# Kernel tuning notes

Measured on AMD Instinct MI355X. Metric: run time of the kernel, lower is better.

## Reference

```python
import jax, jax.numpy as jnp
import numpy as np
import math

# Module constants derived from init_kwargs
DIM1, DIM2 = 32, 32          # n_patches = (512//16, 512//16)
PREFIX = 8                   # num_prefix_tokens
STD = 5.0                    # gauss_std
NUM_HEADS = 12               # orig_attn.num_heads (ViT-B)
EMBED_DIM = 768


def gaussian_window(n1, n2, std):
    # torch linspace(start*c, (start+(n-1))*c, n) == (arange(n)-(n-1)/2)*c
    c = 1.0 / (std * math.sqrt(2.0))
    k1 = (jnp.arange(n1, dtype=jnp.float32) - (n1 - 1) / 2.0) * c
    k2 = (jnp.arange(n2, dtype=jnp.float32) - (n2 - 1) / 2.0) * c
    return jnp.exp(-(k1[:, None] ** 2 + k2[None, :] ** 2))


def attn_addition():
    # Same-padding cross-correlation of per-token delta images with the window
    # collapses to: add[(i,l),(p,q)] = window[i-p+DIM1-1, l-q+DIM2-1]
    win = gaussian_window(2 * DIM1 - 1, 2 * DIM2 - 1, STD)
    i = jnp.arange(DIM1)
    l = jnp.arange(DIM2)
    di = i[:, None] - i[None, :] + (DIM1 - 1)   # [i, p]
    dl = l[:, None] - l[None, :] + (DIM2 - 1)   # [l, q]
    add = win[di[:, None, :, None], dl[None, :, None, :]]  # [i, l, p, q]
    add = add.reshape(DIM1 * DIM2, DIM1 * DIM2)
    # zero rows/cols for prefix tokens (prepended)
    return jnp.pad(add, ((PREFIX, 0), (PREFIX, 0)))


def setup_inputs() -> dict:
    key = jax.random.key(0)
    ks = jax.random.split(key, 5)
    B, N, C = 8, DIM1 * DIM2 + PREFIX, EMBED_DIM
    return {
        "x": jax.random.normal(ks[0], (B, N, C), dtype=jnp.float32),
        "qkv_w": jax.random.normal(ks[1], (3 * C, C), dtype=jnp.float32) * 0.02,
        "qkv_b": jax.random.normal(ks[2], (3 * C,), dtype=jnp.float32) * 0.02,
        "proj_w": jax.random.normal(ks[3], (C, C), dtype=jnp.float32) * 0.02,
        "proj_b": jax.random.normal(ks[4], (C,), dtype=jnp.float32) * 0.02,
    }


def reference(x, qkv_w, qkv_b, proj_w, proj_b):
    B, N, C = x.shape
    H = NUM_HEADS
    hd = C // H
    scale = hd ** (-0.5)
    add = attn_addition()  # [N, N] constant bias

    qkv = x @ qkv_w.T + qkv_b                      # [B, N, 3C]
    q, k, v = jnp.split(qkv, 3, axis=-1)           # q computed but unused (k.k^T attention)
    k = k.reshape(B, N, H, hd)
    v = v.reshape(B, N, H, hd)

    attn = jnp.einsum("bihd,bjhd->bhij", k, k) * scale + add[None, None]
    attn = jax.nn.softmax(attn, axis=-1)
    out = jnp.einsum("bhij,bjhd->bihd", attn, v).reshape(B, N, C)
    out = out @ proj_w.T + proj_b
    return out
```

## Files before the change

### kernel.cpp

```cpp
#include <hip/hip_runtime.h>
#include <stdint.h>

typedef __bf16 bf16;
typedef _Float16 f16;
typedef __bf16 bf16x8 __attribute__((ext_vector_type(8)));
typedef __bf16 bf16x4 __attribute__((ext_vector_type(4)));
typedef float f32x4 __attribute__((ext_vector_type(4)));

#define NSEQ 1032
#define BATCH 8
#define NHEADS 12
#define HD 64
#define CDIM 768
#define MROWS (BATCH * NSEQ)
#define PREFIX 8
#define NJT 17
#define NQ16 72
#define KSTRIDE 1152
#define VSTRIDE 1152
#define KSCALE 0.42466090f

__device__ __forceinline__ unsigned short f2bf_rne(float f) {
    union { float f; uint32_t u; } v; v.f = f;
    uint32_t u = v.u;
    return (unsigned short)((u + 0x7fffu + ((u >> 16) & 1u)) >> 16);
}

__device__ __forceinline__ void gload_lds16(const bf16* g, bf16* l) {
    __builtin_amdgcn_global_load_lds(
        (const __attribute__((address_space(1))) void*)g,
        (__attribute__((address_space(3))) void*)l, 16, 0, 0);
}

__device__ __forceinline__ void cast4(const float* src, bf16* dst, int i) {
    float4 f = ((const float4*)src)[i];
    ushort4 o;
    o.x = f2bf_rne(f.x); o.y = f2bf_rne(f.y);
    o.z = f2bf_rne(f.z); o.w = f2bf_rne(f.w);
    ((ushort4*)dst)[i] = o;
}

__device__ __forceinline__ void bar() {
    asm volatile("s_waitcnt lgkmcnt(0)" ::: "memory");
    __builtin_amdgcn_s_barrier();
    asm volatile("" ::: "memory");
}

#define VMBAR(N) do { \
        asm volatile("s_waitcnt vmcnt(" #N ")" ::: "memory"); \
        __builtin_amdgcn_s_barrier(); \
        asm volatile("" ::: "memory"); \
    } while (0)

__global__ void prep_kernel(const float* __restrict__ x,
                            const float* __restrict__ wkv,
                            const float* __restrict__ pw,
                            bf16* __restrict__ x_bf, bf16* __restrict__ wkv_bf,
                            bf16* __restrict__ pw_bf, float* __restrict__ Bias,
                            bf16* __restrict__ k_bf, bf16* __restrict__ vt_bf) {
    const int N0 = NQ16 * NJT * 1024;
    const int N1 = MROWS * CDIM / 4;
    const int N2 = 2 * CDIM * CDIM / 4;
    const int N3 = CDIM * CDIM / 4;
    const int N4 = BATCH * NHEADS * 120 * 8;
    const int N5 = BATCH * NHEADS * 64 * 15;
    int i = blockIdx.x * blockDim.x + threadIdx.x;
    if (i < N0) {
        int r    = i & 3;
        int l15  = (i >> 2) & 15;
        int quad = (i >> 6) & 3;
        int kt   = (i >> 8) & 3;
        int rest = i >> 10;
        int q16  = rest / NJT;
        int jt   = rest - q16 * NJT;
        int q = q16 * 16 + l15;
        int k = jt * 64 + kt * 16 + quad * 4 + r;
        float v;
        if (k >= NSEQ) v = -65504.f;
        else if (q < PREFIX || q >= NSEQ || k < PREFIX) v = 0.f;
        else {
            int rp = q - PREFIX, cp = k - PREFIX;
            int d1 = (rp >> 5) - (cp >> 5);
            int d2 = (rp & 31) - (cp & 31);
            v = 1.44269504f * __expf(-0.02f * (float)(d1 * d1 + d2 * d2));
        }
        Bias[i] = v;
        return;
    }
    i -= N0;
    if (i < N1) { cast4(x, x_bf, i); return; }
    i -= N1;
    if (i < N2) { cast4(wkv, wkv_bf, i); return; }
    i -= N2;
    if (i < N3) { cast4(pw, pw_bf, i); return; }
    i -= N3;
    if (i < N4) {
        int bh = i / 960, rem = i - bh * 960;
        int row = 1032 + (rem >> 3), ch = rem & 7;
        uint4 z = {0u, 0u, 0u, 0u};
        *(uint4*)&k_bf[((size_t)bh * KSTRIDE + row) * HD + ch * 8] = z;
        return;
    }
    i -= N4;
    if (i < N5) {
        int bh = i / 960, rem = i - bh * 960;
        int d = rem / 15, ch = rem - d * 15;
        uint4 z = {0u, 0u, 0u, 0u};
        *(uint4*)&vt_bf[((size_t)bh * HD + d) * VSTRIDE + 1032 + ch * 8] = z;
    }
}

template<int EPI>
__global__ __launch_bounds__(512) void gemm_nt(
    const bf16* __restrict__ A, const bf16* __restrict__ B,
    const float* __restrict__ bias,
    float* __restrict__ Cout, bf16* __restrict__ Kout, bf16* __restrict__ Vout,
    int M, int N, int K)
{
    __shared__ bf16 sA[2][256 * 32];
    __shared__ bf16 sB[2][128 * 32];
    const int t = threadIdx.x;
    const int w = t >> 6;
    const int l = t & 63;
    const int quad = l >> 4;
    const int l15 = l & 15;
    const int wy = w >> 1, wx = w & 1;

    const int nbx = gridDim.x;
    int id = blockIdx.y * nbx + blockIdx.x;
    {
        int nwg = nbx * gridDim.y;
        int qq = nwg >> 3, rr = nwg & 7;
        int xcd = id & 7, idx = id >> 3;
        id = (xcd < rr) ? (xcd * (qq + 1) + idx)
                        : (rr * (qq + 1) + (xcd - rr) * qq + idx);
    }
    const int m0 = (id / nbx) * 256;
    const int n0 = (id % nbx) * 128;
    const int co = (quad ^ ((l15 >> 1) & 3)) * 8;

    int r0 = t >> 2;            int c0 = (t & 3) ^ ((r0 >> 1) & 3);
    int r1 = 128 + (t >> 2);    int c1 = (t & 3) ^ ((r1 >> 1) & 3);
    int rB = t >> 2;            int cB = (t & 3) ^ ((rB >> 1) & 3);
    int ra0 = m0 + r0; if (ra0 >= M) ra0 = M - 1;
    int ra1 = m0 + r1; if (ra1 >= M) ra1 = M - 1;
    const bf16* gA0 = A + (size_t)ra0 * K + c0 * 8;
    const bf16* gA1 = A + (size_t)ra1 * K + c1 * 8;
    const bf16* gB0 = B + (size_t)(n0 + rB) * K + cB * 8;
    const int oA0 = (w * 64) * 8;
    const int oA1 = (512 + w * 64) * 8;
    const int oB0 = (w * 64) * 8;

    f32x4 acc[4][4] = {};

#define STAGE(BUF) do { \
        gload_lds16(gA0, &sA[BUF][oA0]); gload_lds16(gA1, &sA[BUF][oA1]); \
        gload_lds16(gB0, &sB[BUF][oB0]); \
        gA0 += 32; gA1 += 32; gB0 += 32; \
    } while (0)

#define COMPUTE(BUF) do { \
        bf16x8 af_[4], bq_[4]; \
        _Pragma("unroll") \
        for (int mt = 0; mt < 4; ++mt) \
            af_[mt] = *(const bf16x8*)&sA[BUF][(wy*64 + mt*16 + l15) * 32 + co]; \
        _Pragma("unroll") \
        for (int nt = 0; nt < 4; ++nt) \
            bq_[nt] = *(const bf16x8*)&sB[BUF][(wx*64 + nt*16 + l15) * 32 + co]; \
        _Pragma("unroll") \
        for (int mt = 0; mt < 4; ++mt) \
            _Pragma("unroll") \
            for (int nt = 0; nt < 4; ++nt) \
                acc[mt][nt] = __builtin_amdgcn_mfma_f32_16x16x32_bf16( \
                    af_[mt], bq_[nt], acc[mt][nt], 0, 0, 0); \
    } while (0)

    const int NT = K / 32;
    STAGE(0);
    STAGE(1);
    VMBAR(3);

    #pragma unroll 1
    for (int p = 0; p <= NT - 4; p += 2) {
        COMPUTE(0);
        bar();
        STAGE(0);
        VMBAR(3);
        COMPUTE(1);
        bar();
        STAGE(1);
        VMBAR(3);
    }
    COMPUTE(0);
    VMBAR(0);
    COMPUTE(1);
#undef STAGE
#undef COMPUTE

    if (EPI == 0) {
        #pragma unroll
        for (int mt = 0; mt < 4; ++mt) {
            #pragma unroll
            for (int r = 0; r < 4; ++r) {
                int m = m0 + wy*64 + mt*16 + quad*4 + r;
                if (m >= M) continue;
                #pragma unroll
                for (int nt = 0; nt < 4; ++nt) {
                    int n = n0 + wx*64 + nt*16 + l15;
                    Cout[(size_t)m * N + n] = acc[mt][nt][r] + bias[n];
                }
            }
        }
    } else {
        #pragma unroll
        for (int mt = 0; mt < 4; ++mt) {
            int mb = m0 + wy*64 + mt*16 + quad*4;
            if (mb >= M) continue;
            int b = mb / NSEQ, s = mb % NSEQ;
            #pragma unroll
            for (int nt = 0; nt < 4; ++nt) {
                int n = n0 + wx*64 + nt*16 + l15;
                float bn = bias[n];
                if (n < CDIM) {
                    int h = n >> 6, d = n & 63;
                    bf16* kp = &Kout[(((size_t)(b*NHEADS + h))*KSTRIDE + s)*HD + d];
                    #pragma unroll
                    for (int r = 0; r < 4; ++r)
                        kp[(size_t)r * HD] = (bf16)((acc[mt][nt][r] + bn) * KSCALE);
                } else {
                    int n2 = n - CDIM;
                    int h = n2 >> 6, d = n2 & 63;
                    bf16x4 pv = { (bf16)(acc[mt][nt][0] + bn), (bf16)(acc[mt][nt][1] + bn),
                                  (bf16)(acc[mt][nt][2] + bn), (bf16)(acc[mt][nt][3] + bn) };
                    *(bf16x4*)&Vout[(((size_t)(b*NHEADS + h))*HD + d)*VSTRIDE + s] = pv;
                }
            }
        }
    }
}

__global__ __launch_bounds__(512) void attn_kernel(
    const bf16* __restrict__ Kbuf, const bf16* __restrict__ VTbuf,
    const float* __restrict__ Bias, bf16* __restrict__ Hout)
{
    const int bh = blockIdx.x;
    const int b = bh / NHEADS, h = bh % NHEADS;
    const int q0 = blockIdx.y * 128;
    const bf16* Kh  = Kbuf  + (size_t)bh * KSTRIDE * HD;
    const bf16* VTh = VTbuf + (size_t)bh * HD * VSTRIDE;

    __shared__ bf16 sK[2][64 * 64];
    __shared__ bf16 sVT[2][64 * 64];
    __shared__ bf16 sP[128 * 64];

    const int t = threadIdx.x;
    const int w = t >> 6, l = t & 63, quad = l >> 4, l15 = l & 15;
    const int sw = l15 & 7;

    const int r0 = t >> 3, c0 = t & 7;
    const int dk0 = r0*64 + ((c0 ^ (r0 & 7)) << 3);

    const bf16* pK0 = Kh + (size_t)r0 * HD + c0 * 8;
    const bf16* pV0 = VTh + (size_t)r0 * VSTRIDE + c0 * 8;
    const float* pB = Bias + (size_t)(blockIdx.y*8 + w) * NJT * 1024 + quad*64 + l15*4;

    bf16x8 qf[2];
    {
        int row = q0 + w*16 + l15;
        #pragma unroll
        for (int ks = 0; ks < 2; ++ks)
            qf[ks] = *(const bf16x8*)&Kh[(size_t)row * HD + ks*32 + quad*8];
    }

    bf16x8 onesb;
    #pragma unroll
    for (int e = 0; e < 8; ++e) onesb[e] = (bf16)1.0f;

    f32x4 Oacc[4] = {};
    f32x4 Lacc = {};
    const int sPr0 = (w*16 + l15) * 64;

    uint4 kva, vva;
    f32x4 bpA[4], bpB[4];

#define PREFETCH_KV() do { \
        kva = *(const uint4*)pK0; \
        vva = *(const uint4*)pV0; \
        pK0 += 64*HD; pV0 += 64; \
    } while (0)

#define PREFETCH_B(BANK) do { \
        _Pragma("unroll") \
        for (int kt = 0; kt < 4; ++kt) \
            BANK[kt] = *(const f32x4*)(pB + kt*256); \
        pB += 1024; \
    } while (0)

#define ITER(CUR, ACC, NEXT) do { \
        *(uint4*)&sK[CUR][dk0] = kva; \
        *(uint4*)&sVT[CUR][dk0] = vva; \
        PREFETCH_KV(); \
        PREFETCH_B(NEXT); \
        bar(); \
        _Pragma("unroll") \
        for (int ks = 0; ks < 2; ++ks) { \
            bf16x8 af[4]; \
            _Pragma("unroll") \
            for (int kt = 0; kt < 4; ++kt) \
                af[kt] = *(const bf16x8*)&sK[CUR][(kt*16 + l15)*64 + (((ks*4 + quad) ^ sw) << 3)]; \
            __builtin_amdgcn_s_setprio(1); \
            _Pragma("unroll") \
            for (int kt = 0; kt < 4; ++kt) \
                ACC[kt] = __builtin_amdgcn_mfma_f32_16x16x32_bf16( \
                    af[kt], qf[ks], ACC[kt], 0, 0, 0); \
            __builtin_amdgcn_s_setprio(0); \
        } \
        _Pragma("unroll") \
        for (int kt = 0; kt < 4; ++kt) { \
            float p0 = __builtin_exp2f(ACC[kt][0]); \
            float p1 = __builtin_exp2f(ACC[kt][1]); \
            float p2 = __builtin_exp2f(ACC[kt][2]); \
            float p3 = __builtin_exp2f(ACC[kt][3]); \
            bf16x4 pv = { (bf16)p0, (bf16)p1, (bf16)p2, (bf16)p3 }; \
            int g = (kt*2 + (quad >> 1)) ^ sw; \
            *(bf16x4*)&sP[sPr0 + g*8 + (quad & 1)*4] = pv; \
        } \
        _Pragma("unroll") \
        for (int ks = 0; ks < 2; ++ks) { \
            bf16x8 bv[4]; \
            _Pragma("unroll") \
            for (int dt = 0; dt < 4; ++dt) \
                bv[dt] = *(const bf16x8*)&sVT[CUR][(dt*16 + l15)*64 + (((ks*4 + quad) ^ sw) << 3)]; \
            __builtin_amdgcn_s_setprio(1); \
            bf16x8 ap = *(const bf16x8*)&sP[sPr0 + (((ks*4 + quad) ^ sw) * 8)]; \
            _Pragma("unroll") \
            for (int dt = 0; dt < 4; ++dt) \
                Oacc[dt] = __builtin_amdgcn_mfma_f32_16x16x32_bf16( \
                    ap, bv[dt], Oacc[dt], 0, 0, 0); \
            Lacc = __builtin_amdgcn_mfma_f32_16x16x32_bf16( \
                ap, onesb, Lacc, 0, 0, 0); \
            __builtin_amdgcn_s_setprio(0); \
        } \
    } while (0)

    PREFETCH_KV();
    PREFETCH_B(bpA);
    ITER(0, bpA, bpB);
    #pragma unroll 1
    for (int it = 0; it < (NJT - 1) / 2; ++it) {
        ITER(1, bpB, bpA);
        ITER(0, bpA, bpB);
    }
#undef ITER
#undef PREFETCH_KV
#undef PREFETCH_B

    #pragma unroll
    for (int r = 0; r < 4; ++r) {
        int g = q0 + w*16 + quad*4 + r;
        if (g >= NSEQ) continue;
        float inv = 1.f / Lacc[r];
        size_t base = ((size_t)(b * NSEQ) + g) * CDIM + h * HD;
        #pragma unroll
        for (int dt = 0; dt < 4; ++dt)
            Hout[base + dt*16 + l15] = (bf16)(Oacc[dt][r] * inv);
    }
}

extern "C" void kernel_launch(void* const* d_in, const int* in_sizes, int n_in,
                              void* d_out, int out_size, void* d_ws, size_t ws_size,
                              hipStream_t stream) {
    const float* x      = (const float*)d_in[0];
    const float* qkv_w  = (const float*)d_in[1];
    const float* qkv_b  = (const float*)d_in[2];
    const float* proj_w = (const float*)d_in[3];
    const float* proj_b = (const float*)d_in[4];
    float* out = (float*)d_out;

    char* ws = (char*)d_ws;
    const size_t XBF_BYTES   = (size_t)MROWS * CDIM * 2;
    const size_t WKV_BYTES   = (size_t)2 * CDIM * CDIM * 2;
    const size_t PW_BYTES    = (size_t)CDIM * CDIM * 2;
    const size_t BIAS_BYTES  = (size_t)NQ16 * NJT * 1024 * 4;
    const size_t KBF_BYTES   = (size_t)BATCH * NHEADS * KSTRIDE * HD * 2;

    bf16*  x_bf   = (bf16*)ws;
    bf16*  wkv_bf = (bf16*)(ws + XBF_BYTES);
    bf16*  pw_bf  = (bf16*)(ws + XBF_BYTES + WKV_BYTES);
    float* bias_t = (float*)(ws + XBF_BYTES + WKV_BYTES + PW_BYTES);
    bf16*  k_bf   = (bf16*)(ws + XBF_BYTES + WKV_BYTES + PW_BYTES + BIAS_BYTES);
    bf16*  vt_bf  = (bf16*)(ws + XBF_BYTES + WKV_BYTES + PW_BYTES + BIAS_BYTES + KBF_BYTES);

    {
        int total = NQ16 * NJT * 1024 + MROWS * CDIM / 4
                  + 2 * CDIM * CDIM / 4 + CDIM * CDIM / 4
                  + BATCH * NHEADS * 120 * 8 + BATCH * NHEADS * 64 * 15;
        prep_kernel<<<dim3((total + 255) / 256), dim3(256), 0, stream>>>(
            x, qkv_w + (size_t)CDIM * CDIM, proj_w, x_bf, wkv_bf, pw_bf, bias_t,
            k_bf, vt_bf);
    }

    {
        dim3 grid(1536 / 128, (MROWS + 255) / 256);
        gemm_nt<1><<<grid, dim3(512), 0, stream>>>(x_bf, wkv_bf, qkv_b + CDIM,
                                                   nullptr, k_bf, vt_bf,
                                                   MROWS, 1536, CDIM);
    }

    {
        dim3 grid(BATCH * NHEADS, 9);
        attn_kernel<<<grid, dim3(512), 0, stream>>>(k_bf, vt_bf, bias_t, x_bf);
    }

    {
        dim3 grid(CDIM / 128, (MROWS + 255) / 256);
        gemm_nt<0><<<grid, dim3(512), 0, stream>>>(x_bf, pw_bf, proj_b,
                                                   out, nullptr, nullptr,
                                                   MROWS, CDIM, CDIM);
    }
}
```

Measured before the change: 200.9 us.

## Rewrite attention with 32x32 MFMA, register-resident P, fp16 bias, async LDS staging

Rewrites the attention kernel so each of four waves owns 32 query rows and uses 32x32x16 bf16 MFMAs. The softmax probabilities are packed to bf16 and rearranged with permlane32 swaps, so they stay in registers instead of round-tripping through shared memory. K/V tiles are now staged with direct global-to-LDS loads, double-buffered, replacing register prefetch and LDS stores. The precomputed bias table is stored as fp16 in the new accumulator layout, halving its bandwidth at some precision cost. Block size drops from 512 to 256 threads.

New measurement: 210.8 us. 1.05x slower.

```diff
diff --git a/kernel.cpp b/kernel.cpp
--- a/kernel.cpp
+++ b/kernel.cpp
@@ -6,6 +6,10 @@
 typedef __bf16 bf16x8 __attribute__((ext_vector_type(8)));
 typedef __bf16 bf16x4 __attribute__((ext_vector_type(4)));
 typedef float f32x4 __attribute__((ext_vector_type(4)));
+typedef float f32x16 __attribute__((ext_vector_type(16)));
+typedef _Float16 f16x8 __attribute__((ext_vector_type(8)));
+typedef unsigned int u32x4 __attribute__((ext_vector_type(4)));
+typedef unsigned int uint2v __attribute__((ext_vector_type(2)));
 
 #define NSEQ 1032
 #define BATCH 8
@@ -15,7 +19,7 @@
 #define MROWS (BATCH * NSEQ)
 #define PREFIX 8
 #define NJT 17
-#define NQ16 72
+#define NQ32 36
 #define KSTRIDE 1152
 #define VSTRIDE 1152
 #define KSCALE 0.42466090f
@@ -30,6 +34,12 @@
     __builtin_amdgcn_global_load_lds(
         (const __attribute__((address_space(1))) void*)g,
         (__attribute__((address_space(3))) void*)l, 16, 0, 0);
+}
+
+__device__ __forceinline__ unsigned cvtpk(float lo, float hi) {
+    unsigned r;
+    asm volatile("v_cvt_pk_bf16_f32 %0, %1, %2" : "=v"(r) : "v"(lo), "v"(hi));
+    return r;
 }
 
 __device__ __forceinline__ void cast4(const float* src, bf16* dst, int i) {
@@ -56,9 +66,9 @@
                             const float* __restrict__ wkv,
                             const float* __restrict__ pw,
                             bf16* __restrict__ x_bf, bf16* __restrict__ wkv_bf,
-                            bf16* __restrict__ pw_bf, float* __restrict__ Bias,
+                            bf16* __restrict__ pw_bf, f16* __restrict__ Bias,
                             bf16* __restrict__ k_bf, bf16* __restrict__ vt_bf) {
-    const int N0 = NQ16 * NJT * 1024;
+    const int N0 = NQ32 * NJT * 2048;
     const int N1 = MROWS * CDIM / 4;
     const int N2 = 2 * CDIM * CDIM / 4;
     const int N3 = CDIM * CDIM / 4;
@@ -66,15 +76,14 @@
     const int N5 = BATCH * NHEADS * 64 * 15;
     int i = blockIdx.x * blockDim.x + threadIdx.x;
     if (i < N0) {
-        int r    = i & 3;
-        int l15  = (i >> 2) & 15;
-        int quad = (i >> 6) & 3;
-        int kt   = (i >> 8) & 3;
-        int rest = i >> 10;
-        int q16  = rest / NJT;
-        int jt   = rest - q16 * NJT;
-        int q = q16 * 16 + l15;
-        int k = jt * 64 + kt * 16 + quad * 4 + r;
+        int reg  = i & 15;
+        int lane = (i >> 4) & 63;
+        int kt   = (i >> 10) & 1;
+        int rest = i >> 11;
+        int grp  = rest / NJT;
+        int jt   = rest - grp * NJT;
+        int q = grp * 32 + (lane & 31);
+        int k = jt * 64 + kt * 32 + (reg & 3) + 8 * (reg >> 2) + 4 * (lane >> 5);
         float v;
         if (k >= NSEQ) v = -65504.f;
         else if (q < PREFIX || q >= NSEQ || k < PREFIX) v = 0.f;
@@ -84,7 +93,7 @@
             int d2 = (rp & 31) - (cp & 31);
             v = 1.44269504f * __expf(-0.02f * (float)(d1 * d1 + d2 * d2));
         }
-        Bias[i] = v;
+        Bias[i] = (f16)v;
         return;
     }
     i -= N0;
@@ -239,9 +248,9 @@
     }
 }
 
-__global__ __launch_bounds__(512) void attn_kernel(
+__global__ __launch_bounds__(256) void attn_kernel(
     const bf16* __restrict__ Kbuf, const bf16* __restrict__ VTbuf,
-    const float* __restrict__ Bias, bf16* __restrict__ Hout)
+    const f16* __restrict__ Bias, bf16* __restrict__ Hout)
 {
     const int bh = blockIdx.x;
     const int b = bh / NHEADS, h = bh % NHEADS;
@@ -251,119 +260,140 @@
 
     __shared__ bf16 sK[2][64 * 64];
     __shared__ bf16 sVT[2][64 * 64];
-    __shared__ bf16 sP[128 * 64];
 
     const int t = threadIdx.x;
-    const int w = t >> 6, l = t & 63, quad = l >> 4, l15 = l & 15;
-    const int sw = l15 & 7;
-
-    const int r0 = t >> 3, c0 = t & 7;
-    const int dk0 = r0*64 + ((c0 ^ (r0 & 7)) << 3);
-
-    const bf16* pK0 = Kh + (size_t)r0 * HD + c0 * 8;
-    const bf16* pV0 = VTh + (size_t)r0 * VSTRIDE + c0 * 8;
-    const float* pB = Bias + (size_t)(blockIdx.y*8 + w) * NJT * 1024 + quad*64 + l15*4;
-
-    bf16x8 qf[2];
-    {
-        int row = q0 + w*16 + l15;
+    const int w = t >> 6, l = t & 63;
+    const int l31 = l & 31, hi = l >> 5;
+
+    const int srow = t >> 3;
+    const int sch  = (t & 7) ^ (srow & 7);
+    const bf16* gK0 = Kh  + (size_t)srow * HD + sch * 8;
+    const bf16* gK1 = Kh  + (size_t)(srow + 32) * HD + sch * 8;
+    const bf16* gV0 = VTh + (size_t)srow * VSTRIDE + sch * 8;
+    const bf16* gV1 = VTh + (size_t)(srow + 32) * VSTRIDE + sch * 8;
+    const int ldst = w * 512;
+
+    const f16* pB = Bias + ((size_t)(blockIdx.y * 4 + w) * NJT) * 2048 + l * 16;
+
+    bf16x8 qf[4];
+    {
+        int row = q0 + w * 32 + l31;
         #pragma unroll
-        for (int ks = 0; ks < 2; ++ks)
-            qf[ks] = *(const bf16x8*)&Kh[(size_t)row * HD + ks*32 + quad*8];
+        for (int ks = 0; ks < 4; ++ks)
+            qf[ks] = *(const bf16x8*)&Kh[(size_t)row * HD + ks * 16 + hi * 8];
     }
 
     bf16x8 onesb;
     #pragma unroll
     for (int e = 0; e < 8; ++e) onesb[e] = (bf16)1.0f;
 
-    f32x4 Oacc[4] = {};
-    f32x4 Lacc = {};
-    const int sPr0 = (w*16 + l15) * 64;
-
-    uint4 kva, vva;
-    f32x4 bpA[4], bpB[4];
-
-#define PREFETCH_KV() do { \
-        kva = *(const uint4*)pK0; \
-        vva = *(const uint4*)pV0; \
-        pK0 += 64*HD; pV0 += 64; \
-    } while (0)
-
-#define PREFETCH_B(BANK) do { \
-        _Pragma("unroll") \
-        for (int kt = 0; kt < 4; ++kt) \
-            BANK[kt] = *(const f32x4*)(pB + kt*256); \
-        pB += 1024; \
-    } while (0)
-
-#define ITER(CUR, ACC, NEXT) do { \
-        *(uint4*)&sK[CUR][dk0] = kva; \
-        *(uint4*)&sVT[CUR][dk0] = vva; \
-        PREFETCH_KV(); \
-        PREFETCH_B(NEXT); \
-        bar(); \
-        _Pragma("unroll") \
-        for (int ks = 0; ks < 2; ++ks) { \
-            bf16x8 af[4]; \
-            _Pragma("unroll") \
-            for (int kt = 0; kt < 4; ++kt) \
-                af[kt] = *(const bf16x8*)&sK[CUR][(kt*16 + l15)*64 + (((ks*4 + quad) ^ sw) << 3)]; \
+    f32x16 Oacc0 = {}, Oacc1 = {}, Lacc = {};
+    f16x8 bpf[4];
+
+#define PREFETCH_B() do { \
+        bpf[0] = *(const f16x8*)(pB); \
+        bpf[1] = *(const f16x8*)(pB + 8); \
+        bpf[2] = *(const f16x8*)(pB + 1024); \
+        bpf[3] = *(const f16x8*)(pB + 1032); \
+        pB += 2048; \
+    } while (0)
+
+#define STAGE(BUF) do { \
+        gload_lds16(gK0, &sK[BUF][ldst]); \
+        gload_lds16(gK1, &sK[BUF][2048 + ldst]); \
+        gload_lds16(gV0, &sVT[BUF][ldst]); \
+        gload_lds16(gV1, &sVT[BUF][2048 + ldst]); \
+        gK0 += 64 * HD; gK1 += 64 * HD; gV0 += 64; gV1 += 64; \
+    } while (0)
+
+#define PACK(ACC, FA, FB) do { \
+        float px[16]; \
+        _Pragma("unroll") \
+        for (int r_ = 0; r_ < 16; ++r_) px[r_] = __builtin_exp2f(ACC[r_]); \
+        unsigned pb0 = cvtpk(px[0], px[1]),   pb1 = cvtpk(px[2], px[3]); \
+        unsigned pa0 = cvtpk(px[4], px[5]),   pa1 = cvtpk(px[6], px[7]); \
+        uint2v s0 = __builtin_amdgcn_permlane32_swap(pb0, pa0, false, false); \
+        uint2v s1 = __builtin_amdgcn_permlane32_swap(pb1, pa1, false, false); \
+        u32x4 fa_ = { s0.x, s1.x, s0.y, s1.y }; \
+        FA = *(bf16x8*)&fa_; \
+        unsigned pc0 = cvtpk(px[8], px[9]),   pc1 = cvtpk(px[10], px[11]); \
+        unsigned pd0 = cvtpk(px[12], px[13]), pd1 = cvtpk(px[14], px[15]); \
+        uint2v s2 = __builtin_amdgcn_permlane32_swap(pc0, pd0, false, false); \
+        uint2v s3 = __builtin_amdgcn_permlane32_swap(pc1, pd1, false, false); \
+        u32x4 fb_ = { s2.x, s3.x, s2.y, s3.y }; \
+        FB = *(bf16x8*)&fb_; \
+    } while (0)
+
+#define COMPUTE(BUF) do { \
+        f32x16 a0, a1; \
+        _Pragma("unroll") \
+        for (int r_ = 0; r_ < 16; ++r_) { \
+            a0[r_] = (float)bpf[r_ >> 3][r_ & 7]; \
+            a1[r_] = (float)bpf[2 + (r_ >> 3)][r_ & 7]; \
+        } \
+        PREFETCH_B(); \
+        _Pragma("unroll") \
+        for (int ks = 0; ks < 4; ++ks) { \
+            int c_ = ((ks * 2 + hi) ^ (l31 & 7)) * 8; \
+            bf16x8 af0 = *(const bf16x8*)&sK[BUF][l31 * 64 + c_]; \
+            bf16x8 af1 = *(const bf16x8*)&sK[BUF][2048 + l31 * 64 + c_]; \
             __builtin_amdgcn_s_setprio(1); \
-            _Pragma("unroll") \
-            for (int kt = 0; kt < 4; ++kt) \
-                ACC[kt] = __builtin_amdgcn_mfma_f32_16x16x32_bf16( \
-                    af[kt], qf[ks], ACC[kt], 0, 0, 0); \
+            a0 = __builtin_amdgcn_mfma_f32_32x32x16_bf16(af0, qf[ks], a0, 0, 0, 0); \
+            a1 = __builtin_amdgcn_mfma_f32_32x32x16_bf16(af1, qf[ks], a1, 0, 0, 0); \
             __builtin_amdgcn_s_setprio(0); \
         } \
-        _Pragma("unroll") \
-        for (int kt = 0; kt < 4; ++kt) { \
-            float p0 = __builtin_exp2f(ACC[kt][0]); \
-            float p1 = __builtin_exp2f(ACC[kt][1]); \
-            float p2 = __builtin_exp2f(ACC[kt][2]); \
-            float p3 = __builtin_exp2f(ACC[kt][3]); \
-            bf16x4 pv = { (bf16)p0, (bf16)p1, (bf16)p2, (bf16)p3 }; \
-            int g = (kt*2 + (quad >> 1)) ^ sw; \
-            *(bf16x4*)&sP[sPr0 + g*8 + (quad & 1)*4] = pv; \
-        } \
-        _Pragma("unroll") \
-        for (int ks = 0; ks < 2; ++ks) { \
-            bf16x8 bv[4]; \
-            _Pragma("unroll") \
-            for (int dt = 0; dt < 4; ++dt) \
-                bv[dt] = *(const bf16x8*)&sVT[CUR][(dt*16 + l15)*64 + (((ks*4 + quad) ^ sw) << 3)]; \
+        bf16x8 pf0, pf1, pf2, pf3; \
+        PACK(a0, pf0, pf1); \
+        PACK(a1, pf2, pf3); \
+        bf16x8 pfr[4] = { pf0, pf1, pf2, pf3 }; \
+        _Pragma("unroll") \
+        for (int js = 0; js < 4; ++js) { \
+            int c_ = ((js * 2 + hi) ^ (l31 & 7)) * 8; \
+            bf16x8 bv0 = *(const bf16x8*)&sVT[BUF][l31 * 64 + c_]; \
+            bf16x8 bv1 = *(const bf16x8*)&sVT[BUF][2048 + l31 * 64 + c_]; \
             __builtin_amdgcn_s_setprio(1); \
-            bf16x8 ap = *(const bf16x8*)&sP[sPr0 + (((ks*4 + quad) ^ sw) * 8)]; \
-            _Pragma("unroll") \
-            for (int dt = 0; dt < 4; ++dt) \
-                Oacc[dt] = __builtin_amdgcn_mfma_f32_16x16x32_bf16( \
-                    ap, bv[dt], Oacc[dt], 0, 0, 0); \
-            Lacc = __builtin_amdgcn_mfma_f32_16x16x32_bf16( \
-                ap, onesb, Lacc, 0, 0, 0); \
+            Oacc0 = __builtin_amdgcn_mfma_f32_32x32x16_bf16(pfr[js], bv0, Oacc0, 0, 0, 0); \
+            Oacc1 = __builtin_amdgcn_mfma_f32_32x32x16_bf16(pfr[js], bv1, Oacc1, 0, 0, 0); \
+            Lacc  = __builtin_amdgcn_mfma_f32_32x32x16_bf16(pfr[js], onesb, Lacc, 0, 0, 0); \
             __builtin_amdgcn_s_setprio(0); \
         } \
     } while (0)
 
-    PREFETCH_KV();
-    PREFETCH_B(bpA);
-    ITER(0, bpA, bpB);
+#define ITER(BUF) do { \
+        COMPUTE(BUF); \
+        bar(); \
+        STAGE(BUF); \
+        VMBAR(4); \
+    } while (0)
+
+    PREFETCH_B();
+    STAGE(0);
+    STAGE(1);
+    VMBAR(4);
+
+    ITER(0);
     #pragma unroll 1
-    for (int it = 0; it < (NJT - 1) / 2; ++it) {
-        ITER(1, bpB, bpA);
-        ITER(0, bpA, bpB);
-    }
+    for (int it = 0; it < 7; ++it) {
+        ITER(1);
+        ITER(0);
+    }
+    COMPUTE(1);
+    VMBAR(0);
+    COMPUTE(0);
 #undef ITER
-#undef PREFETCH_KV
+#undef COMPUTE
+#undef PACK
+#undef STAGE
 #undef PREFETCH_B
 
     #pragma unroll
-    for (int r = 0; r < 4; ++r) {
-        int g = q0 + w*16 + quad*4 + r;
-        if (g >= NSEQ) continue;
+    for (int r = 0; r < 16; ++r) {
+        int q = q0 + w * 32 + (r & 3) + 8 * (r >> 2) + 4 * hi;
+        if (q >= NSEQ) continue;
         float inv = 1.f / Lacc[r];
-        size_t base = ((size_t)(b * NSEQ) + g) * CDIM + h * HD;
-        #pragma unroll
-        for (int dt = 0; dt < 4; ++dt)
-            Hout[base + dt*16 + l15] = (bf16)(Oacc[dt][r] * inv);
+        size_t base = ((size_t)(b * NSEQ) + q) * CDIM + h * HD + l31;
+        Hout[base]      = (bf16)(Oacc0[r] * inv);
+        Hout[base + 32] = (bf16)(Oacc1[r] * inv);
     }
 }
 
@@ -381,18 +411,18 @@
     const size_t XBF_BYTES   = (size_t)MROWS * CDIM * 2;
     const size_t WKV_BYTES   = (size_t)2 * CDIM * CDIM * 2;
     const size_t PW_BYTES    = (size_t)CDIM * CDIM * 2;
-    const size_t BIAS_BYTES  = (size_t)NQ16 * NJT * 1024 * 4;
+    const size_t BIAS_BYTES  = (size_t)NQ32 * NJT * 2048 * 2;
     const size_t KBF_BYTES   = (size_t)BATCH * NHEADS * KSTRIDE * HD * 2;
 
-    bf16*  x_bf   = (bf16*)ws;
-    bf16*  wkv_bf = (bf16*)(ws + XBF_BYTES);
-    bf16*  pw_bf  = (bf16*)(ws + XBF_BYTES + WKV_BYTES);
-    float* bias_t = (float*)(ws + XBF_BYTES + WKV_BYTES + PW_BYTES);
-    bf16*  k_bf   = (bf16*)(ws + XBF_BYTES + WKV_BYTES + PW_BYTES + BIAS_BYTES);
-    bf16*  vt_bf  = (bf16*)(ws + XBF_BYTES + WKV_BYTES + PW_BYTES + BIAS_BYTES + KBF_BYTES);
-
-    {
-        int total = NQ16 * NJT * 1024 + MROWS * CDIM / 4
+    bf16* x_bf   = (bf16*)ws;
+    bf16* wkv_bf = (bf16*)(ws + XBF_BYTES);
+    bf16* pw_bf  = (bf16*)(ws + XBF_BYTES + WKV_BYTES);
+    f16*  bias_t = (f16*)(ws + XBF_BYTES + WKV_BYTES + PW_BYTES);
+    bf16* k_bf   = (bf16*)(ws + XBF_BYTES + WKV_BYTES + PW_BYTES + BIAS_BYTES);
+    bf16* vt_bf  = (bf16*)(ws + XBF_BYTES + WKV_BYTES + PW_BYTES + BIAS_BYTES + KBF_BYTES);
+
+    {
+        int total = NQ32 * NJT * 2048 + MROWS * CDIM / 4
                   + 2 * CDIM * CDIM / 4 + CDIM * CDIM / 4
                   + BATCH * NHEADS * 120 * 8 + BATCH * NHEADS * 64 * 15;
         prep_kernel<<<dim3((total + 255) / 256), dim3(256), 0, stream>>>(
@@ -409,7 +439,7 @@
 
     {
         dim3 grid(BATCH * NHEADS, 9);
-        attn_kernel<<<grid, dim3(512), 0, stream>>>(k_bf, vt_bf, bias_t, x_bf);
+        attn_kernel<<<grid, dim3(256), 0, stream>>>(k_bf, vt_bf, bias_t, x_bf);
     }
 
     {
```
